# Kernel tuning notes

Measured on AMD Instinct MI355X. Metric: run time of the kernel, lower is better.

The kernel has to match this reference:

```python
import jax, jax.numpy as jnp
import numpy as np

N_E = 512
E_DIM = 128
LEGACY = 0.2
B, T = 64, 1024


def setup_inputs() -> dict:
    key = jax.random.key(0)
    k1, k2 = jax.random.split(key, 2)
    key_soft = jax.random.normal(k1, (B, T, E_DIM), dtype=jnp.float32)
    emb_weight = jax.random.uniform(k2, (N_E + 1, E_DIM), dtype=jnp.float32,
                                    minval=-1.0 / N_E, maxval=1.0 / N_E)
    zero_ts_mask = jnp.zeros((B,), dtype=jnp.bool_)
    return {"key_soft": key_soft, "emb_weight": emb_weight, "zero_ts_mask": zero_ts_mask}


def _neighbor_indices(d, zero_ts_mask, n_e):
    # d: [B, T, n_e+1] (no grad needed; only used for int index selection)
    ind0 = jnp.clip(jnp.argmin(d[:, 0, :], axis=1), 0, n_e - 1)
    ind0 = jnp.where(zero_ts_mask, 0, ind0)

    def step(ind, d_t):  # ind: [B], d_t: [B, n_e+1]
        d_here = jnp.take_along_axis(d_t, ind[:, None], axis=1)[:, 0]
        ind_next = jnp.clip(ind + 1, 0, n_e - 1)
        d_next = jnp.take_along_axis(d_t, ind_next[:, None], axis=1)[:, 0]
        ind_new = jnp.where(d_here <= d_next, ind, ind_next)
        return ind_new, ind_new

    _, rest = jax.lax.scan(step, ind0, jnp.swapaxes(d[:, 1:, :], 0, 1))  # [T-1, B]
    return jnp.concatenate([ind0[None, :], rest], axis=0).T  # [B, T]


def reference(key_soft, emb_weight, zero_ts_mask):
    sg = jax.lax.stop_gradient
    n_e = emb_weight.shape[0] - 1
    b, t, e_dim = key_soft.shape

    # squared-distance matrix: [B, T, n_e+1]
    d = (jnp.sum(key_soft ** 2, axis=-1, keepdims=True)
         + jnp.sum(emb_weight ** 2, axis=1)
         - 2.0 * jnp.einsum('btd,nd->btn', key_soft, emb_weight))
    d_ng = sg(d)

    min_indices = jnp.argmin(d_ng, axis=-1)                 # [B, T] (over full n_e+1)
    enc = _neighbor_indices(d_ng, zero_ts_mask, n_e)        # [B, T]

    key_hard_here = emb_weight[enc]                                  # [B, T, D]
    key_hard_next = emb_weight[jnp.clip(enc + 1, 0, n_e - 1)]        # [B, T, D]
    key_min = emb_weight[min_indices]                                # [B, T, D]

    def vq_loss(kh):
        return (jnp.sum((sg(key_soft) - kh) ** 2, axis=-1)
                + jnp.sum((key_soft - sg(kh)) ** 2, axis=-1) * LEGACY)

    loss_here_base = vq_loss(key_hard_here)
    loss_next_base = vq_loss(key_hard_next)

    energy = (jnp.sum((sg(key_soft) - key_hard_next) ** 2, axis=-1)
              - jnp.sum((sg(key_soft) - key_hard_here) ** 2, axis=-1)
              + (jnp.sum((key_soft - sg(key_hard_next)) ** 2, axis=-1)
                 - jnp.sum((key_soft - sg(key_hard_here)) ** 2, axis=-1)) * LEGACY)

    change = (enc[:, 1:] - enc[:, :-1]) != 0
    same_hard_mask = jnp.where(change, 0.0, 1.0)
    energy_change = (energy[:, 1:] - energy[:, :-1]) * same_hard_mask
    loss_energy_descent = jnp.maximum(energy_change + 1e-06 / n_e,
                                      jnp.zeros_like(energy_change)).mean()
    energy_mean = energy.mean()

    loss_min_indices = vq_loss(key_min)
    loss_min_here = jnp.where(loss_min_indices < loss_here_base, loss_min_indices, 0.0)
    loss_min_next = jnp.where(loss_min_indices < loss_next_base, loss_min_indices, 0.0)

    loss_here = loss_here_base - loss_next_base - loss_min_here
    loss_next = loss_next_base - loss_here_base - loss_min_next

    key_hard = key_soft + sg(key_hard_here - key_soft)  # straight-through

    v = jnp.max(jnp.max(enc, axis=1) - jnp.min(enc, axis=1))
    return (key_hard, enc, v, loss_here, loss_next, energy_mean, loss_energy_descent)
```

## Files before the change

kernel.cpp:

```cpp
#include <hip/hip_runtime.h>
#include <cfloat>
#include <cstdint>

#define B_  64
#define T_  1024
#define D_  128
#define NE  512
#define P_  (B_*T_)

#define O_KH   0
#define O_ENC  (P_*D_)
#define O_V    (O_ENC + P_)
#define O_LH   (O_V + 1)
#define O_LN   (O_LH + P_)
#define O_EM   (O_LN + P_)
#define O_LED  (O_EM + 1)

typedef __attribute__((ext_vector_type(8))) short bf16x8;
typedef __attribute__((ext_vector_type(4))) float floatx4;

__device__ __forceinline__ void pack8(const float4& a, const float4& b,
                                      uint4& h, uint4& l)
{
    float v[8] = {a.x,a.y,a.z,a.w,b.x,b.y,b.z,b.w};
    unsigned hw[4], lw[4];
    #pragma unroll
    for (int e = 0; e < 4; e++) {
        const unsigned ua = __float_as_uint(v[2*e]);
        const unsigned ub = __float_as_uint(v[2*e+1]);
        const float fa = __uint_as_float(ua & 0xffff0000u);
        const float fb = __uint_as_float(ub & 0xffff0000u);
        const unsigned da = __float_as_uint(v[2*e]   - fa);
        const unsigned db = __float_as_uint(v[2*e+1] - fb);
        hw[e] = (ub & 0xffff0000u) | (ua >> 16);
        lw[e] = (db & 0xffff0000u) | (da >> 16);
    }
    h = make_uint4(hw[0],hw[1],hw[2],hw[3]);
    l = make_uint4(lw[0],lw[1],lw[2],lw[3]);
}

__device__ __forceinline__ unsigned long long shflx64(unsigned long long v, int d)
{
    const int lo = __shfl_xor((int)(unsigned)(v & 0xffffffffULL), d);
    const int hi = __shfl_xor((int)(unsigned)(v >> 32), d);
    return ((unsigned long long)(unsigned)hi << 32) | (unsigned)lo;
}

__global__ __launch_bounds__(256) void kE(const float* __restrict__ emb,
                                          float* __restrict__ sq)
{
    const int w = threadIdx.x >> 6, lane = threadIdx.x & 63;
    const int r = blockIdx.x * 4 + w;
    if (r > 512) return;
    const float2 e = ((const float2*)(emb + (size_t)r * D_))[lane];
    float s = e.x*e.x + e.y*e.y;
    #pragma unroll
    for (int m = 32; m >= 1; m >>= 1) s += __shfl_xor(s, m);
    if (lane == 0) sq[r] = s;
}

__global__ __launch_bounds__(256) void kF(const float* __restrict__ emb,
                                          unsigned short* __restrict__ ehi,
                                          unsigned short* __restrict__ elo)
{
    const int t = blockIdx.x * 256 + threadIdx.x;
    const int n = t >> 2, kst = t & 3;
    const float4* src = (const float4*)(emb + (size_t)n * D_ + kst * 32);
    #pragma unroll
    for (int q = 0; q < 4; q++) {
        uint4 h, l;
        pack8(src[2*q], src[2*q+1], h, l);
        const size_t f = ((size_t)(n >> 4) * 4 + kst) * 4 + q;
        *(uint4*)(ehi + f*128 + (size_t)(n & 15)*8) = h;
        *(uint4*)(elo + f*128 + (size_t)(n & 15)*8) = l;
    }
}

__global__ __launch_bounds__(256) void kA(const float* __restrict__ ks,
                                          const float* __restrict__ sq,
                                          const unsigned short* __restrict__ ehi,
                                          const unsigned short* __restrict__ elo,
                                          unsigned long long* __restrict__ bits,
                                          float* __restrict__ minv,
                                          int* __restrict__ mini)
{
    __shared__ unsigned short Bhi[16*64*8];
    __shared__ unsigned short Blo[16*64*8];
    __shared__ float sF[8][64];

    const int tid  = threadIdx.x;
    const int lane = tid & 63;
    const int wv   = tid >> 6;
    const int m    = lane & 15;
    const int q    = lane >> 4;
    const int p0   = blockIdx.x * 64;

    {
        const int row = tid >> 2;
        const int kh  = tid & 3;
        const float4* src = (const float4*)(ks + (size_t)(p0 + row) * D_ + kh * 32);
        #pragma unroll
        for (int g = 0; g < 4; g++) {
            uint4 h, l;
            pack8(src[2*g], src[2*g+1], h, l);
            const int kq = kh*4 + g;
            *(uint4*)&Bhi[(kq*64 + row)*8] = h;
            *(uint4*)&Blo[(kq*64 + row)*8] = l;
        }
    }
    __syncthreads();

    unsigned long long wsave[2][4];
    float s33save[2][4];

    for (int cc = 0; cc < 2; cc++) {
        const int ch = wv + cc*4;
        const int nb = ch * 64;

        floatx4 acc[4][4];
        #pragma unroll
        for (int i = 0; i < 4; i++)
            #pragma unroll
            for (int j = 0; j < 4; j++)
                #pragma unroll
                for (int r = 0; r < 4; r++) acc[i][j][r] = 0.f;

        #pragma unroll 1
        for (int kst = 0; kst < 4; kst++) {
            bf16x8 ah[4], al[4], bh[4], bl[4];
            #pragma unroll
            for (int i = 0; i < 4; i++) {
                const size_t f = ((size_t)(ch*4 + i) * 4 + kst) * 4 + q;
                ah[i] = *(const bf16x8*)(ehi + f*128 + (size_t)m*8);
                al[i] = *(const bf16x8*)(elo + f*128 + (size_t)m*8);
            }
            const int kq = kst*4 + q;
            #pragma unroll
            for (int j = 0; j < 4; j++) {
                bh[j] = *(const bf16x8*)&Bhi[(kq*64 + j*16 + m)*8];
                bl[j] = *(const bf16x8*)&Blo[(kq*64 + j*16 + m)*8];
            }
            #pragma unroll
            for (int i = 0; i < 4; i++)
                #pragma unroll
                for (int j = 0; j < 4; j++)
                    acc[i][j] = __builtin_amdgcn_mfma_f32_16x16x32_bf16(ah[i], bh[j], acc[i][j], 0, 0, 0);
            #pragma unroll
            for (int i = 0; i < 4; i++)
                #pragma unroll
                for (int j = 0; j < 4; j++)
                    acc[i][j] = __builtin_amdgcn_mfma_f32_16x16x32_bf16(ah[i], bl[j], acc[i][j], 0, 0, 0);
            #pragma unroll
            for (int i = 0; i < 4; i++)
                #pragma unroll
                for (int j = 0; j < 4; j++)
                    acc[i][j] = __builtin_amdgcn_mfma_f32_16x16x32_bf16(al[i], bh[j], acc[i][j], 0, 0, 0);
        }

        float sa[4][4];
        #pragma unroll
        for (int i = 0; i < 4; i++) {
            const float4 s4 = *(const float4*)(sq + nb + i*16 + q*4);
            sa[i][0]=s4.x; sa[i][1]=s4.y; sa[i][2]=s4.z; sa[i][3]=s4.w;
        }
        #pragma unroll
        for (int j = 0; j < 4; j++) {
            float S[4][4];
            #pragma unroll
            for (int i = 0; i < 4; i++)
                #pragma unroll
                for (int r = 0; r < 4; r++)
                    S[i][r] = fmaf(-2.f, acc[i][j][r], sa[i][r]);

            float nq[4], ni[4];
            #pragma unroll
            for (int i = 0; i < 4; i++) nq[i] = __shfl_down(S[i][0], 16);
            #pragma unroll
            for (int i = 0; i < 3; i++) ni[i] = __shfl(S[i+1][0], m);
            ni[3] = 0.f;

            unsigned long long w = 0;
            #pragma unroll
            for (int i = 0; i < 4; i++) {
                #pragma unroll
                for (int r = 0; r < 3; r++)
                    w |= (unsigned long long)(S[i][r] <= S[i][r+1]) << (16*i + 4*q + r);
                if (!(i == 3 && q == 3)) {
                    const float nxt = (q < 3) ? nq[i] : ni[i];
                    w |= (unsigned long long)(S[i][3] <= nxt) << (16*i + 4*q + 3);
                }
            }
            w |= shflx64(w, 16);
            w |= shflx64(w, 32);
            wsave[cc][j]   = w;
            s33save[cc][j] = S[3][3];
            if (q == 0) sF[ch][j*16 + m] = S[0][0];

            float mv = S[0][0]; int mi_ = nb + q*4;
            #pragma unroll
            for (int i = 0; i < 4; i++)
                #pragma unroll
                for (int r = 0; r < 4; r++) {
                    if (i == 0 && r == 0) continue;
                    const int nid = nb + 16*i + 4*q + r;
                    if (S[i][r] < mv) { mv = S[i][r]; mi_ = nid; }
                }
            #pragma unroll
            for (int d = 16; d <= 32; d <<= 1) {
                const float v2 = __shfl_xor(mv, d);
                const int   i2 = __shfl_xor(mi_, d);
                if (v2 < mv || (v2 == mv && i2 < mi_)) { mv = v2; mi_ = i2; }
            }
            const size_t pg = (size_t)(p0 + j*16 + m);
            if (q == 0) {
                minv[pg*8 + ch] = mv;
                mini[pg*8 + ch] = mi_;
            }
        }
    }
    __syncthreads();

    #pragma unroll
    for (int cc = 0; cc < 2; cc++) {
        const int ch = wv + cc*4;
        #pragma unroll
        for (int j = 0; j < 4; j++) {
            const float s33 = __shfl(s33save[cc][j], 48 + m);
            bool b63 = true;
            if (ch < 7) b63 = (s33 <= sF[ch+1][j*16 + m]);
            const unsigned long long w = wsave[cc][j]
                                       | ((unsigned long long)b63 << 63);
            const size_t pg = (size_t)(p0 + j*16 + m);
            if (q == 0) bits[pg*8 + ch] = w;
        }
    }
}

__global__ __launch_bounds__(64) void kB(const float* __restrict__ ks,
                                         const float* __restrict__ emb,
                                         const unsigned char* __restrict__ mask,
                                         const unsigned long long* __restrict__ bits,
                                         const float* __restrict__ minv,
                                         const int* __restrict__ mini,
                                         int* __restrict__ enci,
                                         float* __restrict__ out)
{
    const int b    = blockIdx.x;
    const int lane = threadIdx.x;
    const size_t p0 = (size_t)b * T_;

    const float2 e = ((const float2*)(emb + (size_t)512*D_))[lane];
    const float2 k = ((const float2*)(ks  + p0*D_))[lane];
    float s5 = e.x*(e.x - 2.f*k.x) + e.y*(e.y - 2.f*k.y);
    #pragma unroll
    for (int m = 32; m >= 1; m >>= 1) s5 += __shfl_xor(s5, m);

    float mv; int mi;
    if (lane < 8)       { mv = minv[p0*8 + lane]; mi = mini[p0*8 + lane]; }
    else if (lane == 8) { mv = s5; mi = 512; }
    else                { mv = FLT_MAX; mi = 0x7fffffff; }
    #pragma unroll
    for (int m = 32; m >= 1; m >>= 1) {
        float v2 = __shfl_xor(mv, m);
        int   i2 = __shfl_xor(mi, m);
        if (v2 < mv || (v2 == mv && i2 < mi)) { mv = v2; mi = i2; }
    }
    int cur = (mi < NE) ? mi : NE - 1;
    if (mask[b]) cur = 0;
    if (lane == 0) { enci[p0] = cur; out[O_ENC + p0] = (float)cur; }

    for (int t0 = 1; t0 < T_; t0 += 64) {
        const int w0   = cur >> 6;
        const int off0 = cur & 63;
        const int t    = t0 + lane;
        unsigned long long u = ~0ULL;
        if (t < T_) {
            const size_t base = (p0 + t) * 8;
            const unsigned long long a  = bits[base + w0];
            const unsigned long long b2 = (w0 < 7) ? bits[base + w0 + 1] : ~0ULL;
            u = (off0 == 0) ? a : ((a >> off0) | (b2 << (64 - off0)));
        }
        const unsigned ulo = (unsigned)u;
        const unsigned uhi = (unsigned)(u >> 32);

        int doff = 0;
        int myenc = cur;
        #pragma unroll
        for (int j = 0; j < 64; j++) {
            const unsigned slo = (unsigned)__builtin_amdgcn_readlane((int)ulo, j);
            const unsigned shi = (unsigned)__builtin_amdgcn_readlane((int)uhi, j);
            const unsigned long long word = ((unsigned long long)shi << 32) | slo;
            const int bit = (int)((word >> doff) & 1ULL);
            doff += 1 - bit;
            if (lane == j) myenc = cur + doff;
        }
        cur += doff;
        if (t < T_) {
            enci[p0 + t] = myenc;
            out[O_ENC + p0 + t] = (float)myenc;
        }
    }
}

__global__ __launch_bounds__(256) void kC(const float* __restrict__ ks,
                                          const float* __restrict__ emb,
                                          const int* __restrict__ enci,
                                          const float* __restrict__ minv,
                                          const int* __restrict__ mini,
                                          float* __restrict__ out,
                                          float* __restrict__ energy)
{
    const int lane = threadIdx.x & 63;
    const size_t p = (size_t)blockIdx.x * 4 + (threadIdx.x >> 6);

    const float2 k  = ((const float2*)(ks + p*D_))[lane];
    const int eh = enci[p];
    const int en = (eh + 1 < NE) ? eh + 1 : NE - 1;
    const float2 Eh = ((const float2*)(emb + (size_t)eh*D_))[lane];
    const float2 En = ((const float2*)(emb + (size_t)en*D_))[lane];
    const float2 E5 = ((const float2*)(emb + (size_t)512*D_))[lane];

    float ph  = Eh.x*(Eh.x - 2.f*k.x) + Eh.y*(Eh.y - 2.f*k.y);
    float pn  = En.x*(En.x - 2.f*k.x) + En.y*(En.y - 2.f*k.y);
    float p5  = E5.x*(E5.x - 2.f*k.x) + E5.y*(E5.y - 2.f*k.y);
    float sqk = k.x*k.x + k.y*k.y;
    #pragma unroll
    for (int m = 32; m >= 1; m >>= 1) {
        ph  += __shfl_xor(ph, m);
        pn  += __shfl_xor(pn, m);
        p5  += __shfl_xor(p5, m);
        sqk += __shfl_xor(sqk, m);
    }

    float mv; int mi;
    if (lane < 8)       { mv = minv[p*8 + lane]; mi = mini[p*8 + lane]; }
    else if (lane == 8) { mv = p5; mi = 512; }
    else                { mv = FLT_MAX; mi = 0x7fffffff; }
    #pragma unroll
    for (int m = 32; m >= 1; m >>= 1) {
        float v2 = __shfl_xor(mv, m);
        int   i2 = __shfl_xor(mi, m);
        if (v2 < mv || (v2 == mv && i2 < mi)) { mv = v2; mi = i2; }
    }

    const float2 Em = ((const float2*)(emb + (size_t)mi*D_))[lane];
    float pm = Em.x*(Em.x - 2.f*k.x) + Em.y*(Em.y - 2.f*k.y);
    #pragma unroll
    for (int m = 32; m >= 1; m >>= 1) pm += __shfl_xor(pm, m);

    const float lh = 1.2f * (sqk + ph);
    const float ln = 1.2f * (sqk + pn);
    const float lm = 1.2f * (sqk + pm);
    const float lossh = lh - ln - ((pm < ph) ? lm : 0.f);
    const float lossn = ln - lh - ((pm < pn) ? lm : 0.f);

    float2 kh;
    kh.x = k.x + (Eh.x - k.x);
    kh.y = k.y + (Eh.y - k.y);
    ((float2*)(out + p*D_))[lane] = kh;

    if (lane == 0) {
        out[O_LH + p] = lossh;
        out[O_LN + p] = lossn;
        energy[p] = 1.2f * (pn - ph);
    }
}

__global__ __launch_bounds__(256) void kD1(const float* __restrict__ energy,
                                           const int* __restrict__ enci,
                                           double2* __restrict__ part)
{
    __shared__ double sA[256], sB[256];
    const int p = blockIdx.x * 256 + threadIdx.x;
    const float e = energy[p];
    double se = (double)e;
    double sl = 0.0;
    if ((p & (T_-1)) < T_-1) {
        const float ec = (enci[p+1] == enci[p]) ? (energy[p+1] - e) : 0.f;
        sl = (double)fmaxf(ec + (float)(1e-6/512.0), 0.f);
    }
    sA[threadIdx.x] = se; sB[threadIdx.x] = sl;
    __syncthreads();
    for (int s = 128; s >= 1; s >>= 1) {
        if (threadIdx.x < (unsigned)s) {
            sA[threadIdx.x] += sA[threadIdx.x+s];
            sB[threadIdx.x] += sB[threadIdx.x+s];
        }
        __syncthreads();
    }
    if (threadIdx.x == 0) { part[blockIdx.x] = make_double2(sA[0], sB[0]); }
}

__global__ __launch_bounds__(256) void kD2(const double2* __restrict__ part,
                                           const int* __restrict__ enci,
                                           float* __restrict__ out)
{
    __shared__ double sA[256], sB[256];
    const double2 pv = part[threadIdx.x];
    sA[threadIdx.x] = pv.x; sB[threadIdx.x] = pv.y;
    __syncthreads();
    for (int s = 128; s >= 1; s >>= 1) {
        if (threadIdx.x < (unsigned)s) {
            sA[threadIdx.x] += sA[threadIdx.x+s];
            sB[threadIdx.x] += sB[threadIdx.x+s];
        }
        __syncthreads();
    }
    if (threadIdx.x < 64) {
        int v = enci[(size_t)threadIdx.x*T_ + T_-1] - enci[(size_t)threadIdx.x*T_];
        #pragma unroll
        for (int m = 32; m >= 1; m >>= 1) {
            const int v2 = __shfl_xor(v, m);
            v = (v2 > v) ? v2 : v;
        }
        if (threadIdx.x == 0) {
            out[O_V]   = (float)v;
            out[O_EM]  = (float)(sA[0] / (double)P_);
            out[O_LED] = (float)(sB[0] / (double)(B_*(T_-1)));
        }
    }
}

extern "C" void kernel_launch(void* const* d_in, const int* in_sizes, int n_in,
                              void* d_out, int out_size, void* d_ws, size_t ws_size,
                              hipStream_t stream)
{
    const float* ks  = (const float*)d_in[0];
    const float* emb = (const float*)d_in[1];
    const unsigned char* mask = (const unsigned char*)d_in[2];

    float* out = (float*)d_out;
    char* w = (char*)d_ws;
    unsigned long long* bits = (unsigned long long*)(w);
    float* minv   = (float*)(w + (size_t) 8*1024*1024);
    int*   mini   = (int*)  (w + (size_t)10*1024*1024);
    int*   enci   = (int*)  (w + (size_t)12*1024*1024);
    float* energy = (float*)(w + (size_t)12*1024*1024 + 256*1024);
    float* sq     = (float*)(w + (size_t)12*1024*1024 + 512*1024);
    double2* part = (double2*)(w + (size_t)12*1024*1024 + 516*1024);
    unsigned short* ehi = (unsigned short*)(w + (size_t)12*1024*1024 + 640*1024);
    unsigned short* elo = (unsigned short*)(w + (size_t)12*1024*1024 + 768*1024);

    kE <<<129,  256, 0, stream>>>(emb, sq);
    kF <<<8,    256, 0, stream>>>(emb, ehi, elo);
    kA <<<1024, 256, 0, stream>>>(ks, sq, ehi, elo, bits, minv, mini);
    kB <<<B_,   64,  0, stream>>>(ks, emb, mask, bits, minv, mini, enci, out);
    kC <<<P_/4, 256, 0, stream>>>(ks, emb, enci, minv, mini, out, energy);
    kD1<<<256,  256, 0, stream>>>(energy, enci, part);
    kD2<<<1,    256, 0, stream>>>(part, enci, out);
}
```

Baseline: 214.5 us.

## Split distance GEMM per block, move boundary bits to scan, prefetch scan windows

The codebook squared-norm kernel is folded into the bf16 split-packing kernel, removing one launch. The distance kernel now runs two blocks per 64-pixel tile, each covering four codebook chunks instead of one block looping over eight. This drops the shared-memory boundary exchange and the second barrier, at the cost of packing the query tile twice. Chunk-boundary comparison bits are deferred to the sequential scan kernel using stored first and last distances per chunk. That scan kernel now loads whole 8-word windows with vector loads and double-buffers them, so the next window's memory latency overlaps the serial readlane scan of the current one.

```diff
diff --git a/kernel.cpp b/kernel.cpp
--- a/kernel.cpp
+++ b/kernel.cpp
@@ -18,6 +18,7 @@
 
 typedef __attribute__((ext_vector_type(8))) short bf16x8;
 typedef __attribute__((ext_vector_type(4))) float floatx4;
+typedef unsigned long long u64;
 
 __device__ __forceinline__ void pack8(const float4& a, const float4& b,
                                       uint4& h, uint4& l)
@@ -39,61 +40,59 @@
     l = make_uint4(lw[0],lw[1],lw[2],lw[3]);
 }
 
-__device__ __forceinline__ unsigned long long shflx64(unsigned long long v, int d)
+__device__ __forceinline__ u64 shflx64(u64 v, int d)
 {
     const int lo = __shfl_xor((int)(unsigned)(v & 0xffffffffULL), d);
     const int hi = __shfl_xor((int)(unsigned)(v >> 32), d);
-    return ((unsigned long long)(unsigned)hi << 32) | (unsigned)lo;
-}
-
-__global__ __launch_bounds__(256) void kE(const float* __restrict__ emb,
-                                          float* __restrict__ sq)
-{
-    const int w = threadIdx.x >> 6, lane = threadIdx.x & 63;
-    const int r = blockIdx.x * 4 + w;
-    if (r > 512) return;
-    const float2 e = ((const float2*)(emb + (size_t)r * D_))[lane];
-    float s = e.x*e.x + e.y*e.y;
-    #pragma unroll
-    for (int m = 32; m >= 1; m >>= 1) s += __shfl_xor(s, m);
-    if (lane == 0) sq[r] = s;
+    return ((u64)(unsigned)hi << 32) | (unsigned)lo;
 }
 
 __global__ __launch_bounds__(256) void kF(const float* __restrict__ emb,
                                           unsigned short* __restrict__ ehi,
-                                          unsigned short* __restrict__ elo)
+                                          unsigned short* __restrict__ elo,
+                                          float* __restrict__ sq)
 {
     const int t = blockIdx.x * 256 + threadIdx.x;
     const int n = t >> 2, kst = t & 3;
     const float4* src = (const float4*)(emb + (size_t)n * D_ + kst * 32);
-    #pragma unroll
-    for (int q = 0; q < 4; q++) {
+    float ss = 0.f;
+    #pragma unroll
+    for (int g = 0; g < 4; g++) {
+        const float4 a = src[2*g], b = src[2*g+1];
+        ss += a.x*a.x + a.y*a.y + a.z*a.z + a.w*a.w
+            + b.x*b.x + b.y*b.y + b.z*b.z + b.w*b.w;
         uint4 h, l;
-        pack8(src[2*q], src[2*q+1], h, l);
-        const size_t f = ((size_t)(n >> 4) * 4 + kst) * 4 + q;
-        *(uint4*)(ehi + f*128 + (size_t)(n & 15)*8) = h;
-        *(uint4*)(elo + f*128 + (size_t)(n & 15)*8) = l;
-    }
+        pack8(a, b, h, l);
+        const int f = ((n >> 4) * 4 + kst) * 4 + g;
+        *(uint4*)(ehi + (size_t)f*128 + (size_t)(n & 15)*8) = h;
+        *(uint4*)(elo + (size_t)f*128 + (size_t)(n & 15)*8) = l;
+    }
+    ss += __shfl_xor(ss, 1);
+    ss += __shfl_xor(ss, 2);
+    if (kst == 0) sq[n] = ss;
 }
 
 __global__ __launch_bounds__(256) void kA(const float* __restrict__ ks,
                                           const float* __restrict__ sq,
                                           const unsigned short* __restrict__ ehi,
                                           const unsigned short* __restrict__ elo,
-                                          unsigned long long* __restrict__ bits,
+                                          u64* __restrict__ bits,
+                                          float* __restrict__ sfirst,
+                                          float* __restrict__ slast,
                                           float* __restrict__ minv,
                                           int* __restrict__ mini)
 {
     __shared__ unsigned short Bhi[16*64*8];
     __shared__ unsigned short Blo[16*64*8];
-    __shared__ float sF[8][64];
 
     const int tid  = threadIdx.x;
     const int lane = tid & 63;
     const int wv   = tid >> 6;
     const int m    = lane & 15;
     const int q    = lane >> 4;
-    const int p0   = blockIdx.x * 64;
+    const int p0   = (blockIdx.x >> 1) * 64;
+    const int ch   = (blockIdx.x & 1) * 4 + wv;
+    const int nb   = ch * 64;
 
     {
         const int row = tid >> 2;
@@ -110,136 +109,119 @@
     }
     __syncthreads();
 
-    unsigned long long wsave[2][4];
-    float s33save[2][4];
-
-    for (int cc = 0; cc < 2; cc++) {
-        const int ch = wv + cc*4;
-        const int nb = ch * 64;
-
-        floatx4 acc[4][4];
+    floatx4 acc[4][4];
+    #pragma unroll
+    for (int i = 0; i < 4; i++)
+        #pragma unroll
+        for (int j = 0; j < 4; j++)
+            #pragma unroll
+            for (int r = 0; r < 4; r++) acc[i][j][r] = 0.f;
+
+    #pragma unroll 1
+    for (int kst = 0; kst < 4; kst++) {
+        bf16x8 ah[4], al[4], bh[4], bl[4];
+        #pragma unroll
+        for (int i = 0; i < 4; i++) {
+            const int f = ((ch*4 + i) * 4 + kst) * 4 + q;
+            const int off = f*128 + m*8;
+            ah[i] = *(const bf16x8*)(ehi + off);
+            al[i] = *(const bf16x8*)(elo + off);
+        }
+        const int kq = kst*4 + q;
+        #pragma unroll
+        for (int j = 0; j < 4; j++) {
+            bh[j] = *(const bf16x8*)&Bhi[(kq*64 + j*16 + m)*8];
+            bl[j] = *(const bf16x8*)&Blo[(kq*64 + j*16 + m)*8];
+        }
         #pragma unroll
         for (int i = 0; i < 4; i++)
             #pragma unroll
             for (int j = 0; j < 4; j++)
-                #pragma unroll
-                for (int r = 0; r < 4; r++) acc[i][j][r] = 0.f;
-
-        #pragma unroll 1
-        for (int kst = 0; kst < 4; kst++) {
-            bf16x8 ah[4], al[4], bh[4], bl[4];
-            #pragma unroll
-            for (int i = 0; i < 4; i++) {
-                const size_t f = ((size_t)(ch*4 + i) * 4 + kst) * 4 + q;
-                ah[i] = *(const bf16x8*)(ehi + f*128 + (size_t)m*8);
-                al[i] = *(const bf16x8*)(elo + f*128 + (size_t)m*8);
+                acc[i][j] = __builtin_amdgcn_mfma_f32_16x16x32_bf16(ah[i], bh[j], acc[i][j], 0, 0, 0);
+        #pragma unroll
+        for (int i = 0; i < 4; i++)
+            #pragma unroll
+            for (int j = 0; j < 4; j++)
+                acc[i][j] = __builtin_amdgcn_mfma_f32_16x16x32_bf16(ah[i], bl[j], acc[i][j], 0, 0, 0);
+        #pragma unroll
+        for (int i = 0; i < 4; i++)
+            #pragma unroll
+            for (int j = 0; j < 4; j++)
+                acc[i][j] = __builtin_amdgcn_mfma_f32_16x16x32_bf16(al[i], bh[j], acc[i][j], 0, 0, 0);
+    }
+
+    float sa[4][4];
+    #pragma unroll
+    for (int i = 0; i < 4; i++) {
+        const float4 s4 = *(const float4*)(sq + nb + i*16 + q*4);
+        sa[i][0]=s4.x; sa[i][1]=s4.y; sa[i][2]=s4.z; sa[i][3]=s4.w;
+    }
+    #pragma unroll
+    for (int j = 0; j < 4; j++) {
+        float S[4][4];
+        #pragma unroll
+        for (int i = 0; i < 4; i++)
+            #pragma unroll
+            for (int r = 0; r < 4; r++)
+                S[i][r] = fmaf(-2.f, acc[i][j][r], sa[i][r]);
+
+        float nq[4], ni[4];
+        #pragma unroll
+        for (int i = 0; i < 4; i++) nq[i] = __shfl_down(S[i][0], 16);
+        #pragma unroll
+        for (int i = 0; i < 3; i++) ni[i] = __shfl(S[i+1][0], m);
+        ni[3] = 0.f;
+
+        u64 w = 0;
+        #pragma unroll
+        for (int i = 0; i < 4; i++) {
+            #pragma unroll
+            for (int r = 0; r < 3; r++)
+                w |= (u64)(S[i][r] <= S[i][r+1]) << (16*i + 4*q + r);
+            if (!(i == 3 && q == 3)) {
+                const float nxt = (q < 3) ? nq[i] : ni[i];
+                w |= (u64)(S[i][3] <= nxt) << (16*i + 4*q + 3);
             }
-            const int kq = kst*4 + q;
-            #pragma unroll
-            for (int j = 0; j < 4; j++) {
-                bh[j] = *(const bf16x8*)&Bhi[(kq*64 + j*16 + m)*8];
-                bl[j] = *(const bf16x8*)&Blo[(kq*64 + j*16 + m)*8];
+        }
+        if (ch == 7 && q == 3) w |= 1ULL << 63;
+        w |= shflx64(w, 16);
+        w |= shflx64(w, 32);
+
+        float mv = S[0][0]; int mi_ = nb + q*4;
+        #pragma unroll
+        for (int i = 0; i < 4; i++)
+            #pragma unroll
+            for (int r = 0; r < 4; r++) {
+                if (i == 0 && r == 0) continue;
+                const int nid = nb + 16*i + 4*q + r;
+                if (S[i][r] < mv) { mv = S[i][r]; mi_ = nid; }
             }
-            #pragma unroll
-            for (int i = 0; i < 4; i++)
-                #pragma unroll
-                for (int j = 0; j < 4; j++)
-                    acc[i][j] = __builtin_amdgcn_mfma_f32_16x16x32_bf16(ah[i], bh[j], acc[i][j], 0, 0, 0);
-            #pragma unroll
-            for (int i = 0; i < 4; i++)
-                #pragma unroll
-                for (int j = 0; j < 4; j++)
-                    acc[i][j] = __builtin_amdgcn_mfma_f32_16x16x32_bf16(ah[i], bl[j], acc[i][j], 0, 0, 0);
-            #pragma unroll
-            for (int i = 0; i < 4; i++)
-                #pragma unroll
-                for (int j = 0; j < 4; j++)
-                    acc[i][j] = __builtin_amdgcn_mfma_f32_16x16x32_bf16(al[i], bh[j], acc[i][j], 0, 0, 0);
-        }
-
-        float sa[4][4];
-        #pragma unroll
-        for (int i = 0; i < 4; i++) {
-            const float4 s4 = *(const float4*)(sq + nb + i*16 + q*4);
-            sa[i][0]=s4.x; sa[i][1]=s4.y; sa[i][2]=s4.z; sa[i][3]=s4.w;
-        }
-        #pragma unroll
-        for (int j = 0; j < 4; j++) {
-            float S[4][4];
-            #pragma unroll
-            for (int i = 0; i < 4; i++)
-                #pragma unroll
-                for (int r = 0; r < 4; r++)
-                    S[i][r] = fmaf(-2.f, acc[i][j][r], sa[i][r]);
-
-            float nq[4], ni[4];
-            #pragma unroll
-            for (int i = 0; i < 4; i++) nq[i] = __shfl_down(S[i][0], 16);
-            #pragma unroll
-            for (int i = 0; i < 3; i++) ni[i] = __shfl(S[i+1][0], m);
-            ni[3] = 0.f;
-
-            unsigned long long w = 0;
-            #pragma unroll
-            for (int i = 0; i < 4; i++) {
-                #pragma unroll
-                for (int r = 0; r < 3; r++)
-                    w |= (unsigned long long)(S[i][r] <= S[i][r+1]) << (16*i + 4*q + r);
-                if (!(i == 3 && q == 3)) {
-                    const float nxt = (q < 3) ? nq[i] : ni[i];
-                    w |= (unsigned long long)(S[i][3] <= nxt) << (16*i + 4*q + 3);
-                }
-            }
-            w |= shflx64(w, 16);
-            w |= shflx64(w, 32);
-            wsave[cc][j]   = w;
-            s33save[cc][j] = S[3][3];
-            if (q == 0) sF[ch][j*16 + m] = S[0][0];
-
-            float mv = S[0][0]; int mi_ = nb + q*4;
-            #pragma unroll
-            for (int i = 0; i < 4; i++)
-                #pragma unroll
-                for (int r = 0; r < 4; r++) {
-                    if (i == 0 && r == 0) continue;
-                    const int nid = nb + 16*i + 4*q + r;
-                    if (S[i][r] < mv) { mv = S[i][r]; mi_ = nid; }
-                }
-            #pragma unroll
-            for (int d = 16; d <= 32; d <<= 1) {
-                const float v2 = __shfl_xor(mv, d);
-                const int   i2 = __shfl_xor(mi_, d);
-                if (v2 < mv || (v2 == mv && i2 < mi_)) { mv = v2; mi_ = i2; }
-            }
-            const size_t pg = (size_t)(p0 + j*16 + m);
-            if (q == 0) {
-                minv[pg*8 + ch] = mv;
-                mini[pg*8 + ch] = mi_;
-            }
-        }
-    }
-    __syncthreads();
-
-    #pragma unroll
-    for (int cc = 0; cc < 2; cc++) {
-        const int ch = wv + cc*4;
-        #pragma unroll
-        for (int j = 0; j < 4; j++) {
-            const float s33 = __shfl(s33save[cc][j], 48 + m);
-            bool b63 = true;
-            if (ch < 7) b63 = (s33 <= sF[ch+1][j*16 + m]);
-            const unsigned long long w = wsave[cc][j]
-                                       | ((unsigned long long)b63 << 63);
-            const size_t pg = (size_t)(p0 + j*16 + m);
-            if (q == 0) bits[pg*8 + ch] = w;
-        }
-    }
-}
+        #pragma unroll
+        for (int d = 16; d <= 32; d <<= 1) {
+            const float v2 = __shfl_xor(mv, d);
+            const int   i2 = __shfl_xor(mi_, d);
+            if (v2 < mv || (v2 == mv && i2 < mi_)) { mv = v2; mi_ = i2; }
+        }
+
+        const size_t pg = (size_t)(p0 + j*16 + m);
+        if (q == 0) {
+            bits  [pg*8 + ch] = w;
+            sfirst[pg*8 + ch] = S[0][0];
+            minv  [pg*8 + ch] = mv;
+            mini  [pg*8 + ch] = mi_;
+        }
+        if (q == 3) slast[pg*8 + ch] = S[3][3];
+    }
+}
+
+struct KBwin { u64 W[8]; float F[8]; float L[8]; };
 
 __global__ __launch_bounds__(64) void kB(const float* __restrict__ ks,
                                          const float* __restrict__ emb,
                                          const unsigned char* __restrict__ mask,
-                                         const unsigned long long* __restrict__ bits,
+                                         const u64* __restrict__ bits,
+                                         const float* __restrict__ sfirst,
+                                         const float* __restrict__ slast,
                                          const float* __restrict__ minv,
                                          const int* __restrict__ mini,
                                          int* __restrict__ enci,
@@ -269,36 +251,73 @@
     if (mask[b]) cur = 0;
     if (lane == 0) { enci[p0] = cur; out[O_ENC + p0] = (float)cur; }
 
-    for (int t0 = 1; t0 < T_; t0 += 64) {
+    KBwin wa, wb;
+
+    auto loadwin = [&](KBwin& d, int t0) {
+        const int t = t0 + lane;
+        if (t < T_) {
+            const ulonglong2* bp = (const ulonglong2*)(bits + (p0 + t)*8);
+            const ulonglong2 w01 = bp[0], w23 = bp[1], w45 = bp[2], w67 = bp[3];
+            d.W[0]=w01.x; d.W[1]=w01.y; d.W[2]=w23.x; d.W[3]=w23.y;
+            d.W[4]=w45.x; d.W[5]=w45.y; d.W[6]=w67.x; d.W[7]=w67.y;
+            const float4* fp = (const float4*)(sfirst + (p0 + t)*8);
+            const float4 f0 = fp[0], f1 = fp[1];
+            d.F[0]=f0.x; d.F[1]=f0.y; d.F[2]=f0.z; d.F[3]=f0.w;
+            d.F[4]=f1.x; d.F[5]=f1.y; d.F[6]=f1.z; d.F[7]=f1.w;
+            const float4* lp = (const float4*)(slast + (p0 + t)*8);
+            const float4 l0 = lp[0], l1 = lp[1];
+            d.L[0]=l0.x; d.L[1]=l0.y; d.L[2]=l0.z; d.L[3]=l0.w;
+            d.L[4]=l1.x; d.L[5]=l1.y; d.L[6]=l1.z; d.L[7]=l1.w;
+        } else {
+            #pragma unroll
+            for (int c = 0; c < 8; c++) { d.W[c] = ~0ULL; d.F[c] = 1.f; d.L[c] = 0.f; }
+        }
+    };
+
+    auto scanwin = [&](KBwin& d, int t0) {
+        #pragma unroll
+        for (int c = 0; c < 7; c++)
+            d.W[c] |= (u64)(d.L[c] <= d.F[c+1]) << 63;
+
         const int w0   = cur >> 6;
         const int off0 = cur & 63;
-        const int t    = t0 + lane;
-        unsigned long long u = ~0ULL;
-        if (t < T_) {
-            const size_t base = (p0 + t) * 8;
-            const unsigned long long a  = bits[base + w0];
-            const unsigned long long b2 = (w0 < 7) ? bits[base + w0 + 1] : ~0ULL;
-            u = (off0 == 0) ? a : ((a >> off0) | (b2 << (64 - off0)));
-        }
+        u64 a = d.W[0];
+        #pragma unroll
+        for (int c = 1; c < 8; c++) a = (w0 == c) ? d.W[c] : a;
+        u64 bn = ~0ULL;
+        #pragma unroll
+        for (int c = 1; c < 8; c++) bn = (w0 == c-1) ? d.W[c] : bn;
+        const u64 u = (off0 == 0) ? a : ((a >> off0) | (bn << (64 - off0)));
+
         const unsigned ulo = (unsigned)u;
         const unsigned uhi = (unsigned)(u >> 32);
-
         int doff = 0;
         int myenc = cur;
         #pragma unroll
         for (int j = 0; j < 64; j++) {
             const unsigned slo = (unsigned)__builtin_amdgcn_readlane((int)ulo, j);
             const unsigned shi = (unsigned)__builtin_amdgcn_readlane((int)uhi, j);
-            const unsigned long long word = ((unsigned long long)shi << 32) | slo;
+            const u64 word = ((u64)shi << 32) | slo;
             const int bit = (int)((word >> doff) & 1ULL);
             doff += 1 - bit;
             if (lane == j) myenc = cur + doff;
         }
         cur += doff;
+        const int t = t0 + lane;
         if (t < T_) {
             enci[p0 + t] = myenc;
             out[O_ENC + p0 + t] = (float)myenc;
         }
+    };
+
+    loadwin(wa, 1);
+    #pragma unroll 1
+    for (int wp = 0; wp < 8; wp++) {
+        const int t0a = 1 + wp*128;
+        loadwin(wb, t0a + 64);
+        scanwin(wa, t0a);
+        if (wp < 7) loadwin(wa, t0a + 128);
+        scanwin(wb, t0a + 64);
     }
 }
 
@@ -431,7 +450,9 @@
 
     float* out = (float*)d_out;
     char* w = (char*)d_ws;
-    unsigned long long* bits = (unsigned long long*)(w);
+    u64*   bits   = (u64*)  (w);
+    float* sfirst = (float*)(w + (size_t) 4*1024*1024);
+    float* slast  = (float*)(w + (size_t) 6*1024*1024);
     float* minv   = (float*)(w + (size_t) 8*1024*1024);
     int*   mini   = (int*)  (w + (size_t)10*1024*1024);
     int*   enci   = (int*)  (w + (size_t)12*1024*1024);
@@ -441,10 +462,9 @@
     unsigned short* ehi = (unsigned short*)(w + (size_t)12*1024*1024 + 640*1024);
     unsigned short* elo = (unsigned short*)(w + (size_t)12*1024*1024 + 768*1024);
 
-    kE <<<129,  256, 0, stream>>>(emb, sq);
-    kF <<<8,    256, 0, stream>>>(emb, ehi, elo);
-    kA <<<1024, 256, 0, stream>>>(ks, sq, ehi, elo, bits, minv, mini);
-    kB <<<B_,   64,  0, stream>>>(ks, emb, mask, bits, minv, mini, enci, out);
+    kF <<<8,    256, 0, stream>>>(emb, ehi, elo, sq);
+    kA <<<2048, 256, 0, stream>>>(ks, sq, ehi, elo, bits, sfirst, slast, minv, mini);
+    kB <<<B_,   64,  0, stream>>>(ks, emb, mask, bits, sfirst, slast, minv, mini, enci, out);
     kC <<<P_/4, 256, 0, stream>>>(ks, emb, enci, minv, mini, out, energy);
     kD1<<<256,  256, 0, stream>>>(energy, enci, part);
     kD2<<<1,    256, 0, stream>>>(part, enci, out);
```

After: 197.2 us. 1.09x faster.
